# Optimization experiments

Measured on AMD Instinct MI355X. Metric: run time of the kernel, lower is better.

## Reference

```python
import jax, jax.numpy as jnp
import numpy as np

N = 100000   # nodes
E = 1600000  # edges (before self loops)
IN = 128
H = 64
OUT = 10
G = 256      # graphs in batch
BN_EPS = 1e-5
NEG_SLOPE = 0.2


def setup_inputs() -> dict:
    key = jax.random.key(0)
    ks = jax.random.split(key, 24)
    def p(k, shape, fan_in):
        # glorot-ish init for weights
        s = 1.0 / np.sqrt(fan_in)
        return jax.random.uniform(k, shape, jnp.float32, -s, s)
    inp = {
        "x": jax.random.normal(ks[0], (N, IN), jnp.float32),
        "edge_index": jax.random.randint(ks[1], (2, E), 0, N),
        "batch": jnp.sort(jax.random.randint(ks[2], (N,), 0, G)),
        # GATConv 1 (in -> hidden, heads=1)
        "W1": p(ks[3], (IN, H), IN), "as1": p(ks[4], (H,), H), "ad1": p(ks[5], (H,), H), "b1": jnp.zeros((H,), jnp.float32),
        # GATConv 2 (hidden -> hidden)
        "W2": p(ks[6], (H, H), H), "as2": p(ks[7], (H,), H), "ad2": p(ks[8], (H,), H), "b2": jnp.zeros((H,), jnp.float32),
        # shared BatchNorm1d(hidden) params (bn1 reused twice)
        "bn_g": jnp.ones((H,), jnp.float32), "bn_b": jnp.zeros((H,), jnp.float32),
        # MLP head: hidden->64->16->8->out
        "m1_w": p(ks[9], (H, 64), H), "m1_b": jnp.zeros((64,), jnp.float32),
        "m2_w": p(ks[10], (64, 16), 64), "m2_b": jnp.zeros((16,), jnp.float32),
        "m3_w": p(ks[11], (16, 8), 16), "m3_b": jnp.zeros((8,), jnp.float32),
        "m4_w": p(ks[12], (8, OUT), 8), "m4_b": jnp.zeros((OUT,), jnp.float32),
    }
    return inp


def gat_conv(x, src, dst, W, a_src, a_dst, b, n):
    # PyG GATConv, heads=1, concat=True, negative_slope=0.2
    h = x @ W                                  # [n, H]
    alpha_s = h @ a_src                        # [n]
    alpha_d = h @ a_dst                        # [n]
    e = jax.nn.leaky_relu(alpha_s[src] + alpha_d[dst], NEG_SLOPE)  # [E']
    # segment softmax over incoming edges of each dst node
    emax = jax.ops.segment_max(e, dst, num_segments=n)
    w = jnp.exp(e - emax[dst])
    denom = jax.ops.segment_sum(w, dst, num_segments=n)
    alpha = w / denom[dst]
    out = jax.ops.segment_sum(h[src] * alpha[:, None], dst, num_segments=n)
    return out + b


def batch_norm(x, g, b):
    # training-mode BN over nodes
    m = jnp.mean(x, axis=0)
    v = jnp.mean((x - m) ** 2, axis=0)
    return (x - m) * jax.lax.rsqrt(v + BN_EPS) * g + b


def reference(x, edge_index, batch, W1, as1, ad1, b1, W2, as2, ad2, b2,
              bn_g, bn_b, m1_w, m1_b, m2_w, m2_b, m3_w, m3_b, m4_w, m4_b):
    n = x.shape[0]
    loop = jnp.arange(n, dtype=edge_index.dtype)
    src = jnp.concatenate([edge_index[0], loop])   # add self loops (PyG default)
    dst = jnp.concatenate([edge_index[1], loop])

    h = jax.nn.relu(gat_conv(x, src, dst, W1, as1, ad1, b1, n))
    h = batch_norm(h, bn_g, bn_b)
    h = jax.nn.relu(gat_conv(h, src, dst, W2, as2, ad2, b2, n))
    h = batch_norm(h, bn_g, bn_b)

    # global mean pool per graph
    s = jax.ops.segment_sum(h, batch, num_segments=G)                       # [G, H]
    cnt = jax.ops.segment_sum(jnp.ones((n,), h.dtype), batch, num_segments=G)
    pooled = s / jnp.maximum(cnt, 1.0)[:, None]

    z = jax.nn.relu(pooled @ m1_w + m1_b)
    z = jax.nn.relu(z @ m2_w + m2_b)
    z = jax.nn.relu(z @ m3_w + m3_b)
    return z @ m4_w + m4_b                                                  # [G, OUT]
```

## Files before the change

kernel.cpp:

```cpp
#include <hip/hip_runtime.h>
#include <hip/hip_fp16.h>

#define NN   100000
#define NE   1600000
#define ET   (NE + NN)
#define INF_ 128
#define HID  64
#define NG   256
#define BN_EPS 1e-5f
#define NEG  0.2f

#define BSPAN_LOG 8
#define BSPAN     (1 << BSPAN_LOG)
#define NBUK      ((NN + BSPAN - 1) / BSPAN)
#define BUKCAP    5120
#define P1_EPT    16
#define P1_CHUNK  (256 * P1_EPT)

__device__ __forceinline__ float lrelu(float v) { return v > 0.f ? v : NEG * v; }

__device__ __forceinline__ float readlane_f(float v, int l) {
  return __int_as_float(__builtin_amdgcn_readlane(__float_as_int(v), l));
}

__global__ __launch_bounds__(256) void init_k(
    int* __restrict__ bukcur,
    float* __restrict__ fsum1, float* __restrict__ fsq1,
    float* __restrict__ fsum2, float* __restrict__ fsq2,
    float* __restrict__ pooled, float* __restrict__ cnt) {
  int i = blockIdx.x * 256 + threadIdx.x;
  if (i < NBUK) bukcur[i] = i * BUKCAP;
  if (i < HID) { fsum1[i] = 0.f; fsq1[i] = 0.f; fsum2[i] = 0.f; fsq2[i] = 0.f; }
  if (i < NG * HID) pooled[i] = 0.f;
  if (i < NG) cnt[i] = 0.f;
}

__global__ __launch_bounds__(256) void part1_k(const int* __restrict__ ei,
                                               int* __restrict__ bukcur,
                                               int2* __restrict__ stage) {
  __shared__ int hist[NBUK];
  __shared__ int base[NBUK];
  int t = threadIdx.x;
  for (int b = t; b < NBUK; b += 256) hist[b] = 0;
  __syncthreads();
  int chunk = blockIdx.x * P1_CHUNK;
  int myb[P1_EPT], myr[P1_EPT], mys[P1_EPT], myd[P1_EPT];
#pragma unroll
  for (int it = 0; it < P1_EPT; ++it) {
    int i = chunk + it * 256 + t;
    bool v = i < ET;
    int src = 0, dst = 0;
    if (v) {
      src = i < NE ? ei[i] : i - NE;
      dst = i < NE ? ei[NE + i] : i - NE;
    }
    myb[it] = v ? (dst >> BSPAN_LOG) : -1;
    mys[it] = src;
    myd[it] = dst;
    myr[it] = v ? atomicAdd(&hist[dst >> BSPAN_LOG], 1) : 0;
  }
  __syncthreads();
  for (int b = t; b < NBUK; b += 256)
    base[b] = hist[b] ? atomicAdd(&bukcur[b], hist[b]) : 0;
  __syncthreads();
#pragma unroll
  for (int it = 0; it < P1_EPT; ++it)
    if (myb[it] >= 0)
      stage[base[myb[it]] + myr[it]] = make_int2(mys[it], myd[it]);
}

__global__ __launch_bounds__(512) void bukscan_k(const int* __restrict__ bukcur,
                                                 int* __restrict__ bukbase,
                                                 int* __restrict__ rowptr) {
  __shared__ int sh[512];
  int t = threadIdx.x;
  int c = (t < NBUK) ? (bukcur[t] - t * BUKCAP) : 0;
  sh[t] = c;
  __syncthreads();
  for (int off = 1; off < 512; off <<= 1) {
    int add = (t >= off) ? sh[t - off] : 0;
    __syncthreads();
    sh[t] += add;
    __syncthreads();
  }
  if (t < NBUK) bukbase[t] = sh[t] - c;
  if (t == 0) rowptr[NN] = ET;
}

__global__ __launch_bounds__(256) void part2_k(const int2* __restrict__ stage,
                                               const int* __restrict__ bukcur,
                                               const int* __restrict__ bukbase,
                                               int* __restrict__ rowptr,
                                               int* __restrict__ esrc) {
  __shared__ int lcnt[BSPAN];
  __shared__ int lscan[BSPAN];
  int b = blockIdx.x;
  int node0 = b << BSPAN_LOG;
  int t = threadIdx.x;
  lcnt[t] = 0;
  __syncthreads();
  int s = b * BUKCAP, e = bukcur[b];
  for (int i = s + t; i < e; i += 256)
    atomicAdd(&lcnt[stage[i].y - node0], 1);
  __syncthreads();
  int v = lcnt[t];
  lscan[t] = v;
  __syncthreads();
  for (int off = 1; off < 256; off <<= 1) {
    int add = (t >= off) ? lscan[t - off] : 0;
    __syncthreads();
    lscan[t] += add;
    __syncthreads();
  }
  int excl = bukbase[b] + lscan[t] - v;
  if (node0 + t < NN) rowptr[node0 + t] = excl;
  lcnt[t] = excl;
  __syncthreads();
  for (int i = s + t; i < e; i += 256) {
    int2 p = stage[i];
    int pos = atomicAdd(&lcnt[p.y - node0], 1);
    esrc[pos] = p.x;
  }
}

template <int K, bool STATS>
__global__ __launch_bounds__(256) void gemm_att(
    const float* __restrict__ x,
    const float* __restrict__ fsum, const float* __restrict__ fsq,
    const float* __restrict__ bng, const float* __restrict__ bnb,
    const float* __restrict__ W,
    const float* __restrict__ a_s, const float* __restrict__ a_d,
    __half* __restrict__ h, float* __restrict__ sv_out, float* __restrict__ dv_out) {
  __shared__ float Wl[K * HID];
  __shared__ float cvec[HID];
  __shared__ float scl[HID], shf[HID];
  int tid = threadIdx.x;
  if (tid < HID) {
    cvec[tid] = 0.f;
    if (STATS) {
      float m = fsum[tid] * (1.0f / NN);
      float v = fsq[tid] * (1.0f / NN) - m * m;
      float a = bng[tid] * rsqrtf(v + BN_EPS);
      scl[tid] = a;
      shf[tid] = bnb[tid] - m * a;
    }
  }
  __syncthreads();
  if (STATS) {
    float clocal = 0.f;
    for (int i = tid; i < K * HID; i += 256) {
      int k = i >> 6;
      float w = W[i];
      clocal += shf[k] * w;
      Wl[i] = w * scl[k];
    }
    atomicAdd(&cvec[tid & 63], clocal);
  } else {
    for (int i = tid; i < K * HID; i += 256) Wl[i] = W[i];
  }
  __syncthreads();

  int lane = tid & 63;
  int wid = tid >> 6;
  int row0 = blockIdx.x * 16 + wid * 4;
  int ur = __builtin_amdgcn_readfirstlane(row0);
  const float* xr0 = x + (size_t)ur * K;
  const float* xr1 = xr0 + K;
  const float* xr2 = xr0 + 2 * K;
  const float* xr3 = xr0 + 3 * K;
  float cv = cvec[lane];
  float a0 = cv, a1 = cv, a2 = cv, a3 = cv;
#pragma unroll 4
  for (int k = 0; k < K; k += 4) {
    float4 v0 = *(const float4*)(xr0 + k);
    float4 v1 = *(const float4*)(xr1 + k);
    float4 v2 = *(const float4*)(xr2 + k);
    float4 v3 = *(const float4*)(xr3 + k);
    float w0 = Wl[(k + 0) * HID + lane];
    float w1 = Wl[(k + 1) * HID + lane];
    float w2 = Wl[(k + 2) * HID + lane];
    float w3 = Wl[(k + 3) * HID + lane];
    a0 = fmaf(v0.x, w0, a0); a0 = fmaf(v0.y, w1, a0);
    a0 = fmaf(v0.z, w2, a0); a0 = fmaf(v0.w, w3, a0);
    a1 = fmaf(v1.x, w0, a1); a1 = fmaf(v1.y, w1, a1);
    a1 = fmaf(v1.z, w2, a1); a1 = fmaf(v1.w, w3, a1);
    a2 = fmaf(v2.x, w0, a2); a2 = fmaf(v2.y, w1, a2);
    a2 = fmaf(v2.z, w2, a2); a2 = fmaf(v2.w, w3, a2);
    a3 = fmaf(v3.x, w0, a3); a3 = fmaf(v3.y, w1, a3);
    a3 = fmaf(v3.z, w2, a3); a3 = fmaf(v3.w, w3, a3);
  }

  float asl = a_s[lane], adl = a_d[lane];
  h[(size_t)(row0 + 0) * HID + lane] = __float2half(a0);
  h[(size_t)(row0 + 1) * HID + lane] = __float2half(a1);
  h[(size_t)(row0 + 2) * HID + lane] = __float2half(a2);
  h[(size_t)(row0 + 3) * HID + lane] = __float2half(a3);
  float s0 = a0 * asl, d0 = a0 * adl;
  float s1 = a1 * asl, d1 = a1 * adl;
  float s2 = a2 * asl, d2 = a2 * adl;
  float s3 = a3 * asl, d3 = a3 * adl;
  for (int o = 32; o; o >>= 1) {
    s0 += __shfl_xor(s0, o); d0 += __shfl_xor(d0, o);
    s1 += __shfl_xor(s1, o); d1 += __shfl_xor(d1, o);
    s2 += __shfl_xor(s2, o); d2 += __shfl_xor(d2, o);
    s3 += __shfl_xor(s3, o); d3 += __shfl_xor(d3, o);
  }
  if (lane == 0) {
    sv_out[row0 + 0] = s0; dv_out[row0 + 0] = d0;
    sv_out[row0 + 1] = s1; dv_out[row0 + 1] = d1;
    sv_out[row0 + 2] = s2; dv_out[row0 + 2] = d2;
    sv_out[row0 + 3] = s3; dv_out[row0 + 3] = d3;
  }
}

__device__ __forceinline__ float2 gat_node(
    int node, const int* __restrict__ rowptr, const int* __restrict__ esrc,
    const float* __restrict__ s, const float* __restrict__ d,
    const __half* __restrict__ h, int lane, int half, int fl) {
  int start = rowptr[node], end = rowptr[node + 1];
  int deg = end - start;
  float dn = d[node];
  float2 acc = {0.f, 0.f};
  if (deg <= 64) {
    int j = start + (lane < deg ? lane : 0);
    int sj = esrc[j];
    float e = lrelu(s[sj] + dn);
    float ev = (lane < deg) ? e : -INFINITY;
    float m = ev;
    for (int o = 32; o; o >>= 1) m = fmaxf(m, __shfl_xor(m, o));
    float w = (lane < deg) ? __expf(e - m) : 0.f;
    float wsum = w;
    for (int o = 32; o; o >>= 1) wsum += __shfl_xor(wsum, o);
    float alpha = w / wsum;
    for (int t = 0; t < deg; t += 8) {
#pragma unroll
      for (int i = 0; i < 4; ++i) {
        int e0 = t + 2 * i;
        int p0 = __builtin_amdgcn_readlane(sj, e0);
        int p1 = __builtin_amdgcn_readlane(sj, e0 + 1);
        float a0 = readlane_f(alpha, e0);
        float a1 = readlane_f(alpha, e0 + 1);
        int ps = half ? p1 : p0;
        float aw = half ? a1 : a0;
        float2 hv = __half22float2(*(const __half2*)&h[(size_t)ps * HID + fl]);
        acc.x = fmaf(aw, hv.x, acc.x);
        acc.y = fmaf(aw, hv.y, acc.y);
      }
    }
  } else {
    float m = -INFINITY;
    for (int j = start + lane; j < end; j += 64)
      m = fmaxf(m, lrelu(s[esrc[j]] + dn));
    for (int o = 32; o; o >>= 1) m = fmaxf(m, __shfl_xor(m, o));
    float wsum = 0.f;
    for (int j = start + lane; j < end; j += 64)
      wsum += __expf(lrelu(s[esrc[j]] + dn) - m);
    for (int o = 32; o; o >>= 1) wsum += __shfl_xor(wsum, o);
    float inv = 1.0f / wsum;
    for (int cb = start; cb < end; cb += 64) {
      int cc = min(64, end - cb);
      int j = cb + (lane < cc ? lane : 0);
      int sj = esrc[j];
      float alpha = (lane < cc) ? __expf(lrelu(s[sj] + dn) - m) * inv : 0.f;
      for (int t = 0; t < cc; t += 8) {
#pragma unroll
        for (int i = 0; i < 4; ++i) {
          int e0 = t + 2 * i;
          int p0 = __builtin_amdgcn_readlane(sj, e0);
          int p1 = __builtin_amdgcn_readlane(sj, e0 + 1);
          float a0 = readlane_f(alpha, e0);
          float a1 = readlane_f(alpha, e0 + 1);
          int ps = half ? p1 : p0;
          float aw = half ? a1 : a0;
          float2 hv = __half22float2(*(const __half2*)&h[(size_t)ps * HID + fl]);
          acc.x = fmaf(aw, hv.x, acc.x);
          acc.y = fmaf(aw, hv.y, acc.y);
        }
      }
    }
  }
  acc.x += __shfl_xor(acc.x, 32);
  acc.y += __shfl_xor(acc.y, 32);
  return acc;
}

__global__ __launch_bounds__(256) void gat_agg_k(
    const int* __restrict__ rowptr, const int* __restrict__ esrc,
    const float* __restrict__ s, const float* __restrict__ d,
    const __half* __restrict__ h, const float* __restrict__ bias,
    float* __restrict__ y, float* __restrict__ fsum, float* __restrict__ fsq) {
  __shared__ float lsum[HID], lsq[HID];
  int tid = threadIdx.x;
  if (tid < HID) { lsum[tid] = 0.f; lsq[tid] = 0.f; }
  __syncthreads();
  int lane = tid & 63;
  int half = lane >> 5;
  int fl = (lane & 31) * 2;
  float2 bv = *(const float2*)&bias[fl];
  float2 ls = {0.f, 0.f}, lq = {0.f, 0.f};
  int wave = blockIdx.x * 4 + (tid >> 6);
  int nwaves = gridDim.x * 4;
  for (int node = wave; node < NN; node += nwaves) {
    float2 acc = gat_node(node, rowptr, esrc, s, d, h, lane, half, fl);
    float vx = fmaxf(acc.x + bv.x, 0.f);
    float vy = fmaxf(acc.y + bv.y, 0.f);
    if (half == 0) {
      *(float2*)&y[(size_t)node * HID + fl] = make_float2(vx, vy);
      ls.x += vx; ls.y += vy;
      lq.x += vx * vx; lq.y += vy * vy;
    }
  }
  if (lane < 32) {
    atomicAdd(&lsum[fl + 0], ls.x);
    atomicAdd(&lsum[fl + 1], ls.y);
    atomicAdd(&lsq[fl + 0], lq.x);
    atomicAdd(&lsq[fl + 1], lq.y);
  }
  __syncthreads();
  if (tid < HID) { atomicAdd(&fsum[tid], lsum[tid]); atomicAdd(&fsq[tid], lsq[tid]); }
}

__global__ __launch_bounds__(256) void gat_agg_pool_k(
    const int* __restrict__ rowptr, const int* __restrict__ esrc,
    const float* __restrict__ s, const float* __restrict__ d,
    const __half* __restrict__ h, const float* __restrict__ bias,
    const int* __restrict__ batch, float* __restrict__ pooled,
    float* __restrict__ cnt, float* __restrict__ fsum, float* __restrict__ fsq) {
  __shared__ float lsum[HID], lsq[HID];
  int tid = threadIdx.x;
  if (tid < HID) { lsum[tid] = 0.f; lsq[tid] = 0.f; }
  __syncthreads();
  int lane = tid & 63;
  int half = lane >> 5;
  int fl = (lane & 31) * 2;
  float2 bv = *(const float2*)&bias[fl];
  float2 ls = {0.f, 0.f}, lq = {0.f, 0.f};
  int wave = blockIdx.x * 4 + (tid >> 6);
  int nwaves = gridDim.x * 4;
  int per = (NN + nwaves - 1) / nwaves;
  int lo = wave * per, hi = min(lo + per, NN);
  if (lo < hi) {
    int g = batch[lo];
    float2 pacc = {0.f, 0.f};
    float c = 0.f;
    for (int node = lo; node < hi; ++node) {
      int bg = batch[node];
      if (bg != g) {
        if (half == 0) {
          atomicAdd(&pooled[g * HID + fl + 0], pacc.x);
          atomicAdd(&pooled[g * HID + fl + 1], pacc.y);
        }
        if (lane == 0) atomicAdd(&cnt[g], c);
        g = bg; pacc.x = 0.f; pacc.y = 0.f; c = 0.f;
      }
      float2 acc = gat_node(node, rowptr, esrc, s, d, h, lane, half, fl);
      float vx = fmaxf(acc.x + bv.x, 0.f);
      float vy = fmaxf(acc.y + bv.y, 0.f);
      pacc.x += vx; pacc.y += vy; c += 1.f;
      if (half == 0) {
        ls.x += vx; ls.y += vy;
        lq.x += vx * vx; lq.y += vy * vy;
      }
    }
    if (half == 0) {
      atomicAdd(&pooled[g * HID + fl + 0], pacc.x);
      atomicAdd(&pooled[g * HID + fl + 1], pacc.y);
    }
    if (lane == 0) atomicAdd(&cnt[g], c);
  }
  if (lane < 32) {
    atomicAdd(&lsum[fl + 0], ls.x);
    atomicAdd(&lsum[fl + 1], ls.y);
    atomicAdd(&lsq[fl + 0], lq.x);
    atomicAdd(&lsq[fl + 1], lq.y);
  }
  __syncthreads();
  if (tid < HID) { atomicAdd(&fsum[tid], lsum[tid]); atomicAdd(&fsq[tid], lsq[tid]); }
}

__global__ __launch_bounds__(64) void mlp_head(
    const float* __restrict__ pooled, const float* __restrict__ cnt,
    const float* __restrict__ fsum, const float* __restrict__ fsq,
    const float* __restrict__ bng, const float* __restrict__ bnb,
    const float* __restrict__ m1w, const float* __restrict__ m1b,
    const float* __restrict__ m2w, const float* __restrict__ m2b,
    const float* __restrict__ m3w, const float* __restrict__ m3b,
    const float* __restrict__ m4w, const float* __restrict__ m4b,
    float* __restrict__ out) {
  __shared__ float p[64], z1[64], z2[16], z3[8];
  int g = blockIdx.x, f = threadIdx.x;
  float m = fsum[f] * (1.0f / NN);
  float v = fsq[f] * (1.0f / NN) - m * m;
  float a = bng[f] * rsqrtf(v + BN_EPS);
  float c = bnb[f] - m * a;
  float cv = fmaxf(cnt[g], 1.0f);
  p[f] = a * pooled[g * 64 + f] / cv + c;
  __syncthreads();
  float a1 = m1b[f];
  for (int k = 0; k < 64; ++k) a1 += p[k] * m1w[k * 64 + f];
  z1[f] = fmaxf(a1, 0.f);
  __syncthreads();
  if (f < 16) {
    float a2 = m2b[f];
    for (int k = 0; k < 64; ++k) a2 += z1[k] * m2w[k * 16 + f];
    z2[f] = fmaxf(a2, 0.f);
  }
  __syncthreads();
  if (f < 8) {
    float a3 = m3b[f];
    for (int k = 0; k < 16; ++k) a3 += z2[k] * m3w[k * 8 + f];
    z3[f] = fmaxf(a3, 0.f);
  }
  __syncthreads();
  if (f < 10) {
    float a4 = m4b[f];
    for (int k = 0; k < 8; ++k) a4 += z3[k] * m4w[k * 10 + f];
    out[g * 10 + f] = a4;
  }
}

extern "C" void kernel_launch(void* const* d_in, const int* in_sizes, int n_in,
                              void* d_out, int out_size, void* d_ws, size_t ws_size,
                              hipStream_t stream) {
  const float* x   = (const float*)d_in[0];
  const int*   ei  = (const int*)d_in[1];
  const int*   bat = (const int*)d_in[2];
  const float* W1  = (const float*)d_in[3];
  const float* as1 = (const float*)d_in[4];
  const float* ad1 = (const float*)d_in[5];
  const float* b1  = (const float*)d_in[6];
  const float* W2  = (const float*)d_in[7];
  const float* as2 = (const float*)d_in[8];
  const float* ad2 = (const float*)d_in[9];
  const float* b2  = (const float*)d_in[10];
  const float* bng = (const float*)d_in[11];
  const float* bnb = (const float*)d_in[12];
  const float* m1w = (const float*)d_in[13];
  const float* m1b = (const float*)d_in[14];
  const float* m2w = (const float*)d_in[15];
  const float* m2b = (const float*)d_in[16];
  const float* m3w = (const float*)d_in[17];
  const float* m3b = (const float*)d_in[18];
  const float* m4w = (const float*)d_in[19];
  const float* m4b = (const float*)d_in[20];
  float* out = (float*)d_out;

  float* ws = (float*)d_ws;
  size_t off = 0;
  __half* hbuf = (__half*)(ws + off); off += (size_t)NN * HID / 2;
  float* ybuf = ws + off; off += (size_t)NN * HID;
  float* sbuf = ws + off; off += NN;
  float* dbuf = ws + off; off += NN;
  int* rowptr = (int*)(ws + off); off += NN + 1;
  int* esrc   = (int*)(ws + off); off += ET;
  int* bukcur = (int*)(ws + off); off += NBUK;
  int* bukbase = (int*)(ws + off); off += NBUK;
  float* fsum1 = ws + off; off += HID;
  float* fsq1  = ws + off; off += HID;
  float* fsum2 = ws + off; off += HID;
  float* fsq2  = ws + off; off += HID;
  float* pooled = ws + off; off += (size_t)NG * HID;
  float* cnt  = ws + off; off += NG;
  int2* stage = (int2*)ybuf;

  dim3 b256(256);
  const int gemmGrid = NN / 16;
  const int p1Grid = (ET + P1_CHUNK - 1) / P1_CHUNK;
  const int aggGrid = 2048;

  init_k<<<(NG * HID + 255) / 256, b256, 0, stream>>>(bukcur, fsum1, fsq1,
                                                      fsum2, fsq2, pooled, cnt);
  part1_k<<<p1Grid, b256, 0, stream>>>(ei, bukcur, stage);
  bukscan_k<<<1, 512, 0, stream>>>(bukcur, bukbase, rowptr);
  part2_k<<<NBUK, b256, 0, stream>>>(stage, bukcur, bukbase, rowptr, esrc);

  gemm_att<INF_, false><<<gemmGrid, b256, 0, stream>>>(
      x, nullptr, nullptr, nullptr, nullptr, W1, as1, ad1, hbuf, sbuf, dbuf);
  gat_agg_k<<<aggGrid, b256, 0, stream>>>(rowptr, esrc, sbuf, dbuf, hbuf, b1,
                                          ybuf, fsum1, fsq1);

  gemm_att<HID, true><<<gemmGrid, b256, 0, stream>>>(
      ybuf, fsum1, fsq1, bng, bnb, W2, as2, ad2, hbuf, sbuf, dbuf);
  gat_agg_pool_k<<<aggGrid, b256, 0, stream>>>(rowptr, esrc, sbuf, dbuf, hbuf,
                                               b2, bat, pooled, cnt, fsum2, fsq2);

  mlp_head<<<NG, 64, 0, stream>>>(pooled, cnt, fsum2, fsq2, bng, bnb,
                                  m1w, m1b, m2w, m2b, m3w, m3b, m4w, m4b, out);
}
```

Measured before the change: 386.9 us.

## Process two nodes per wave with half-wave aggregation for low-degree pairs

Each wave now handles a pair of nodes. When both have degree at most 32, each 32-lane half computes softmax and aggregation for its own node, using shuffles instead of readlanes. Otherwise it falls back to the full-wave path and runs the two nodes one after the other. The aim is to stop wasting half the wave on the low-degree nodes that dominate this graph (average degree about 17), at the cost of divergence and a slower serialized path for high-degree pairs. Gather offsets also switch to 32-bit unsigned indexing.

```diff
diff --git a/kernel.cpp b/kernel.cpp
--- a/kernel.cpp
+++ b/kernel.cpp
@@ -213,7 +213,37 @@
   }
 }
 
-__device__ __forceinline__ float2 gat_node(
+__device__ __forceinline__ float2 gat_node_half(
+    int node, int start, int deg, const int* __restrict__ esrc,
+    const float* __restrict__ s, const float* __restrict__ d,
+    const __half* __restrict__ h, int lane32, int base, int fl) {
+  float dn = d[node];
+  int j = start + (lane32 < deg ? lane32 : 0);
+  int sj = esrc[j];
+  float e = lrelu(s[sj] + dn);
+  float ev = (lane32 < deg) ? e : -INFINITY;
+  float m = ev;
+  for (int o = 16; o; o >>= 1) m = fmaxf(m, __shfl_xor(m, o));
+  float w = (lane32 < deg) ? __expf(e - m) : 0.f;
+  float wsum = w;
+  for (int o = 16; o; o >>= 1) wsum += __shfl_xor(wsum, o);
+  float alpha = w / wsum;
+  float2 acc = {0.f, 0.f};
+  for (int t = 0; t < deg; t += 4) {
+#pragma unroll
+    for (int i = 0; i < 4; ++i) {
+      int p = __shfl(sj, base + t + i);
+      float a = __shfl(alpha, base + t + i);
+      unsigned off = ((unsigned)p << 6) + fl;
+      float2 hv = __half22float2(*(const __half2*)&h[off]);
+      acc.x = fmaf(a, hv.x, acc.x);
+      acc.y = fmaf(a, hv.y, acc.y);
+    }
+  }
+  return acc;
+}
+
+__device__ float2 gat_node_full(
     int node, const int* __restrict__ rowptr, const int* __restrict__ esrc,
     const float* __restrict__ s, const float* __restrict__ d,
     const __half* __restrict__ h, int lane, int half, int fl) {
@@ -242,7 +272,8 @@
         float a1 = readlane_f(alpha, e0 + 1);
         int ps = half ? p1 : p0;
         float aw = half ? a1 : a0;
-        float2 hv = __half22float2(*(const __half2*)&h[(size_t)ps * HID + fl]);
+        unsigned off = ((unsigned)ps << 6) + fl;
+        float2 hv = __half22float2(*(const __half2*)&h[off]);
         acc.x = fmaf(aw, hv.x, acc.x);
         acc.y = fmaf(aw, hv.y, acc.y);
       }
@@ -272,7 +303,8 @@
           float a1 = readlane_f(alpha, e0 + 1);
           int ps = half ? p1 : p0;
           float aw = half ? a1 : a0;
-          float2 hv = __half22float2(*(const __half2*)&h[(size_t)ps * HID + fl]);
+          unsigned off = ((unsigned)ps << 6) + fl;
+          float2 hv = __half22float2(*(const __half2*)&h[off]);
           acc.x = fmaf(aw, hv.x, acc.x);
           acc.y = fmaf(aw, hv.y, acc.y);
         }
@@ -282,6 +314,24 @@
   acc.x += __shfl_xor(acc.x, 32);
   acc.y += __shfl_xor(acc.y, 32);
   return acc;
+}
+
+__device__ __forceinline__ float2 gat_pair(
+    int nA, const int* __restrict__ rowptr, const int* __restrict__ esrc,
+    const float* __restrict__ s, const float* __restrict__ d,
+    const __half* __restrict__ h, int lane, int half, int lane32, int fl) {
+  int nB = nA + 1;
+  int sA = rowptr[nA], sB = rowptr[nB], eB = rowptr[nB + 1];
+  int degA = sB - sA, degB = eB - sB;
+  if (degA <= 32 && degB <= 32) {
+    int node = half ? nB : nA;
+    int start = half ? sB : sA;
+    int deg = half ? degB : degA;
+    return gat_node_half(node, start, deg, esrc, s, d, h, lane32, half << 5, fl);
+  }
+  float2 aA = gat_node_full(nA, rowptr, esrc, s, d, h, lane, half, fl);
+  float2 aB = gat_node_full(nB, rowptr, esrc, s, d, h, lane, half, fl);
+  return half ? aB : aA;
 }
 
 __global__ __launch_bounds__(256) void gat_agg_k(
@@ -295,27 +345,26 @@
   __syncthreads();
   int lane = tid & 63;
   int half = lane >> 5;
-  int fl = (lane & 31) * 2;
+  int lane32 = lane & 31;
+  int fl = lane32 * 2;
   float2 bv = *(const float2*)&bias[fl];
   float2 ls = {0.f, 0.f}, lq = {0.f, 0.f};
   int wave = blockIdx.x * 4 + (tid >> 6);
   int nwaves = gridDim.x * 4;
-  for (int node = wave; node < NN; node += nwaves) {
-    float2 acc = gat_node(node, rowptr, esrc, s, d, h, lane, half, fl);
+  for (int p = wave; p < NN / 2; p += nwaves) {
+    int nA = 2 * p;
+    float2 acc = gat_pair(nA, rowptr, esrc, s, d, h, lane, half, lane32, fl);
     float vx = fmaxf(acc.x + bv.x, 0.f);
     float vy = fmaxf(acc.y + bv.y, 0.f);
-    if (half == 0) {
-      *(float2*)&y[(size_t)node * HID + fl] = make_float2(vx, vy);
-      ls.x += vx; ls.y += vy;
-      lq.x += vx * vx; lq.y += vy * vy;
-    }
-  }
-  if (lane < 32) {
-    atomicAdd(&lsum[fl + 0], ls.x);
-    atomicAdd(&lsum[fl + 1], ls.y);
-    atomicAdd(&lsq[fl + 0], lq.x);
-    atomicAdd(&lsq[fl + 1], lq.y);
-  }
+    int node = nA + half;
+    *(float2*)&y[(size_t)node * HID + fl] = make_float2(vx, vy);
+    ls.x += vx; ls.y += vy;
+    lq.x += vx * vx; lq.y += vy * vy;
+  }
+  atomicAdd(&lsum[fl + 0], ls.x);
+  atomicAdd(&lsum[fl + 1], ls.y);
+  atomicAdd(&lsq[fl + 0], lq.x);
+  atomicAdd(&lsq[fl + 1], lq.y);
   __syncthreads();
   if (tid < HID) { atomicAdd(&fsum[tid], lsum[tid]); atomicAdd(&fsq[tid], lsq[tid]); }
 }
@@ -332,48 +381,42 @@
   __syncthreads();
   int lane = tid & 63;
   int half = lane >> 5;
-  int fl = (lane & 31) * 2;
+  int lane32 = lane & 31;
+  int fl = lane32 * 2;
   float2 bv = *(const float2*)&bias[fl];
   float2 ls = {0.f, 0.f}, lq = {0.f, 0.f};
   int wave = blockIdx.x * 4 + (tid >> 6);
   int nwaves = gridDim.x * 4;
-  int per = (NN + nwaves - 1) / nwaves;
+  int per = (((NN / 2) + nwaves - 1) / nwaves) * 2;
   int lo = wave * per, hi = min(lo + per, NN);
   if (lo < hi) {
-    int g = batch[lo];
+    int g = batch[lo + half];
     float2 pacc = {0.f, 0.f};
     float c = 0.f;
-    for (int node = lo; node < hi; ++node) {
-      int bg = batch[node];
+    for (int nA = lo; nA < hi; nA += 2) {
+      int myn = nA + half;
+      int bg = batch[myn];
       if (bg != g) {
-        if (half == 0) {
-          atomicAdd(&pooled[g * HID + fl + 0], pacc.x);
-          atomicAdd(&pooled[g * HID + fl + 1], pacc.y);
-        }
-        if (lane == 0) atomicAdd(&cnt[g], c);
+        atomicAdd(&pooled[g * HID + fl + 0], pacc.x);
+        atomicAdd(&pooled[g * HID + fl + 1], pacc.y);
+        if (lane32 == 0) atomicAdd(&cnt[g], c);
         g = bg; pacc.x = 0.f; pacc.y = 0.f; c = 0.f;
       }
-      float2 acc = gat_node(node, rowptr, esrc, s, d, h, lane, half, fl);
+      float2 acc = gat_pair(nA, rowptr, esrc, s, d, h, lane, half, lane32, fl);
       float vx = fmaxf(acc.x + bv.x, 0.f);
       float vy = fmaxf(acc.y + bv.y, 0.f);
       pacc.x += vx; pacc.y += vy; c += 1.f;
-      if (half == 0) {
-        ls.x += vx; ls.y += vy;
-        lq.x += vx * vx; lq.y += vy * vy;
-      }
-    }
-    if (half == 0) {
-      atomicAdd(&pooled[g * HID + fl + 0], pacc.x);
-      atomicAdd(&pooled[g * HID + fl + 1], pacc.y);
-    }
-    if (lane == 0) atomicAdd(&cnt[g], c);
-  }
-  if (lane < 32) {
-    atomicAdd(&lsum[fl + 0], ls.x);
-    atomicAdd(&lsum[fl + 1], ls.y);
-    atomicAdd(&lsq[fl + 0], lq.x);
-    atomicAdd(&lsq[fl + 1], lq.y);
-  }
+      ls.x += vx; ls.y += vy;
+      lq.x += vx * vx; lq.y += vy * vy;
+    }
+    atomicAdd(&pooled[g * HID + fl + 0], pacc.x);
+    atomicAdd(&pooled[g * HID + fl + 1], pacc.y);
+    if (lane32 == 0) atomicAdd(&cnt[g], c);
+  }
+  atomicAdd(&lsum[fl + 0], ls.x);
+  atomicAdd(&lsum[fl + 1], ls.y);
+  atomicAdd(&lsq[fl + 0], lq.x);
+  atomicAdd(&lsq[fl + 1], lq.y);
   __syncthreads();
   if (tid < HID) { atomicAdd(&fsum[tid], lsum[tid]); atomicAdd(&fsq[tid], lsq[tid]); }
 }
```

Result: faster. 375.9 us (median of 2 runs) (-2.8%).
